# Kernel optimization log

Hardware: AMD Instinct MI355X
Metric: run time of the kernel (lower is better)

The kernel has to match this reference:

```python
import jax, jax.numpy as jnp
import numpy as np

N, IN_DIM, HEADS, OUT_DIM = 4096, 128, 4, 64
NEG_INF = -9.0e15  # finite mask value, matches torch source


def setup_inputs() -> dict:
    key = jax.random.key(0)
    k1, k2, k3, k4, k5 = jax.random.split(key, 5)
    x = jax.random.normal(k1, (N, IN_DIM), dtype=jnp.float32)
    adj_mask = jax.random.bernoulli(k2, 0.1, (N, N))  # bool, j->i edges
    # xavier-uniform-ish scales
    lim_w = float(np.sqrt(6.0 / (IN_DIM + HEADS * OUT_DIM)))
    W_lin = jax.random.uniform(k3, (IN_DIM, HEADS * OUT_DIM), minval=-lim_w, maxval=lim_w, dtype=jnp.float32)
    lim_a = float(np.sqrt(6.0 / (2 * OUT_DIM + 1)))
    a_src = jax.random.uniform(k4, (OUT_DIM,), minval=-lim_a, maxval=lim_a, dtype=jnp.float32)
    a_dst = jax.random.uniform(k5, (OUT_DIM,), minval=-lim_a, maxval=lim_a, dtype=jnp.float32)
    return {"x": x, "adj_mask": adj_mask, "W_lin": W_lin, "a_src": a_src, "a_dst": a_dst}


def reference(x, adj_mask, W_lin, a_src, a_dst):
    n = x.shape[0]
    h = (x @ W_lin).reshape(n, HEADS, OUT_DIM)           # (N, H, D)
    # att(cat(h_i, h_j)) decomposes linearly: a_src.h_i + a_dst.h_j
    s_i = jnp.einsum("nhd,d->nh", h, a_src)              # (N, H) contribution of dest node i
    s_j = jnp.einsum("nhd,d->nh", h, a_dst)              # (N, H) contribution of source node j
    e = jax.nn.leaky_relu(s_i[:, None, :] + s_j[None, :, :], 0.2)  # (N, N, H)
    e = jnp.where(adj_mask[:, :, None], e, NEG_INF)
    attn = jax.nn.softmax(e, axis=1)                     # softmax over source nodes j
    out = jnp.einsum("ijh,jhd->ihd", attn, h)            # per-head aggregation
    return out.reshape(n, HEADS * OUT_DIM)               # concat=True
```

## Files before the change

### kernel.cpp

```cpp
#include <hip/hip_runtime.h>
#include <math.h>


#define N 4096
#define IN_DIM 128
#define HEADS 4
#define OUT_DIM 64
#define HD 256
#define LOG2E 1.4426950408889634f
#define PSHIFT 8.0f

typedef _Float16 f16x8 __attribute__((ext_vector_type(8)));
typedef __fp16 fp16x2 __attribute__((ext_vector_type(2)));
typedef float f32x4 __attribute__((ext_vector_type(4)));

union F16x8u { fp16x2 h2[4]; f16x8 v; };

#define WS_HB_OFF    0u
#define WS_SSRC_OFF  2097152u
#define WS_SDT_OFF   2162688u
#define WS_BITT_OFF  2228224u
#define WS_HSUM_OFF  4325376u
#define WS_PL_OFF    4329472u
#define WS_PART_OFF  5242880u
#define WS_NEED8     (5242880u + 8u * 4194304u)
#define WS_NEED2     (5242880u + 2u * 4194304u)

__device__ __forceinline__ float lrelu(float v) { return fmaxf(v, 0.2f * v); }

__device__ __forceinline__ unsigned pack_bytes(unsigned v) {
  return (v & 1u) | ((v >> 7) & 2u) | ((v >> 14) & 4u) | ((v >> 21) & 8u);
}

__global__ __launch_bounds__(256) void prep_k(const void* __restrict__ mraw,
                                              unsigned* __restrict__ bits_t,
                                              const float* __restrict__ x,
                                              const float* __restrict__ W,
                                              const float* __restrict__ a_src,
                                              const float* __restrict__ a_dst,
                                              _Float16* __restrict__ hb,
                                              float* __restrict__ s_src,
                                              float* __restrict__ s_dst_t,
                                              float* __restrict__ hsum) {
  if (blockIdx.x < 2048) {
    __shared__ int s_flag;
    if (threadIdx.x == 0) s_flag = 0;
    __syncthreads();
    const unsigned* mw = (const unsigned*)mraw;
    int bad = 0, g = 0;
    for (int i = threadIdx.x; i < 1024; i += 256) {
      unsigned v = mw[i];
      if (v & 0xFEFEFEFEu) bad = 1;
      if (v > 1u) g = 1;
    }
    if (bad || g) atomicOr(&s_flag, (bad ? 1 : 0) | (g ? 2 : 0));
    __syncthreads();
    const bool byte_fmt = ((s_flag & 1) == 0) && ((s_flag & 2) != 0);

    int w = blockIdx.x * 256 + threadIdx.x;
    unsigned ob = 0u;
    if (byte_fmt) {
      const uint4* p = (const uint4*)((const unsigned char*)mraw + (size_t)w * 32u);
      uint4 a = p[0], b = p[1];
      ob  =  pack_bytes(a.x)        | (pack_bytes(a.y) << 4)  | (pack_bytes(a.z) << 8)  | (pack_bytes(a.w) << 12);
      ob |= (pack_bytes(b.x) << 16) | (pack_bytes(b.y) << 20) | (pack_bytes(b.z) << 24) | (pack_bytes(b.w) << 28);
    } else {
      const uint4* p = (const uint4*)((const unsigned*)mraw + (size_t)w * 32u);
#pragma unroll
      for (int k = 0; k < 8; ++k) {
        uint4 v = p[k];
        ob |= (v.x ? 1u : 0u) << (4 * k);
        ob |= (v.y ? 1u : 0u) << (4 * k + 1);
        ob |= (v.z ? 1u : 0u) << (4 * k + 2);
        ob |= (v.w ? 1u : 0u) << (4 * k + 3);
      }
    }
    const int row = w >> 7, jc = w & 127;
    bits_t[((size_t)(row >> 6) * 128 + jc) * 64 + (row & 63)] = ob;
  } else {
    const int i0 = (blockIdx.x - 2048) * 8;
    const int c = threadIdx.x;

    float acc[8];
#pragma unroll
    for (int r = 0; r < 8; ++r) acc[r] = 0.f;

    for (int kk = 0; kk < IN_DIM / 4; ++kk) {
      const int k = kk * 4;
      float w0 = W[(size_t)(k + 0) * HD + c];
      float w1 = W[(size_t)(k + 1) * HD + c];
      float w2 = W[(size_t)(k + 2) * HD + c];
      float w3 = W[(size_t)(k + 3) * HD + c];
#pragma unroll
      for (int r = 0; r < 8; ++r) {
        float4 xv = *(const float4*)(x + (size_t)(i0 + r) * IN_DIM + k);
        acc[r] = fmaf(xv.x, w0, fmaf(xv.y, w1, fmaf(xv.z, w2, fmaf(xv.w, w3, acc[r]))));
      }
    }

    {
      const int head = c >> 6, nt = (c >> 4) & 3, m15 = c & 15;
      const int unit = (head * 128 + (i0 >> 5)) * 4 + nt;
      const int lanep = ((i0 & 31) >> 3) * 16 + m15;
      f16x8 v;
#pragma unroll
      for (int r = 0; r < 8; ++r) v[r] = (_Float16)acc[r];
      *(f16x8*)(hb + (size_t)unit * 512 + lanep * 8) = v;
    }

    {
      float loc = 0.f;
#pragma unroll
      for (int r = 0; r < 8; ++r) loc += acc[r];
      atomicAdd(&hsum[c], loc);
    }

    const int hw = c >> 6, lane = c & 63;
    const float as = a_src[lane], ad = a_dst[lane];
#pragma unroll
    for (int r = 0; r < 8; ++r) {
      float vs = acc[r] * as, vd = acc[r] * ad;
#pragma unroll
      for (int off = 1; off < 64; off <<= 1) {
        vs += __shfl_xor(vs, off);
        vd += __shfl_xor(vd, off);
      }
      if (lane == 0) {
        s_src[(size_t)(i0 + r) * HEADS + hw] = vs * LOG2E;
        s_dst_t[(size_t)hw * N + (i0 + r)] = vd * LOG2E;
      }
    }
  }
}

__global__ __launch_bounds__(512, 4) void gat_aggr(const _Float16* __restrict__ hb,
                                                   const float* __restrict__ s_src,
                                                   const float* __restrict__ s_dst_t,
                                                   const unsigned* __restrict__ bits_t,
                                                   float* __restrict__ accp,
                                                   float* __restrict__ lp,
                                                   int jshift) {
  const int jsplit = 1 << jshift;
  const int jrange = N >> jshift;
  const int chunks = jrange >> 5;
  const int tid = threadIdx.x;
  const int wave = tid >> 6;
  const int lane = tid & 63;
  const int head = wave & 3;
  const int mg = wave >> 2;
  const int m15 = lane & 15;
  const int quad = lane >> 4;
  const int jq = blockIdx.x & (jsplit - 1);
  const int it = blockIdx.x >> jshift;
  const int i0 = it * 64;
  const int rA = i0 + mg * 32 + m15;
  const int rB = rA + 16;

  const float siA = s_src[(size_t)rA * HEADS + head];
  const float siB = s_src[(size_t)rB * HEADS + head];

  const unsigned* mt = bits_t + ((size_t)it * 128 + jq * chunks) * 64 + mg * 32 + m15;
  const float* sjb = s_dst_t + (size_t)head * N + jq * jrange + quad * 8;
  const _Float16* hbp = hb + ((size_t)(head * 128 + jq * chunks) * 4) * 512 + lane * 8;

  f32x4 accA0 = {0.f, 0.f, 0.f, 0.f}, accA1 = accA0, accA2 = accA0, accA3 = accA0;
  f32x4 accB0 = accA0, accB1 = accA0, accB2 = accA0, accB3 = accA0;
  float lA = 0.f, lB = 0.f;

  const int shq = quad * 8;

  for (int c = 0; c < chunks; ++c) {
    const unsigned mwA = mt[c * 64];
    const unsigned mwB = mt[c * 64 + 16];
    const float4 sa = *(const float4*)(sjb + c * 32);
    const float4 sb = *(const float4*)(sjb + c * 32 + 4);

    const f16x8 b0 = *(const f16x8*)(hbp + (size_t)(c * 4 + 0) * 512);
    const f16x8 b1 = *(const f16x8*)(hbp + (size_t)(c * 4 + 1) * 512);
    const f16x8 b2 = *(const f16x8*)(hbp + (size_t)(c * 4 + 2) * 512);
    const f16x8 b3 = *(const f16x8*)(hbp + (size_t)(c * 4 + 3) * 512);

    const unsigned wA = mwA >> shq;
    const unsigned wB = mwB >> shq;
    const float sjs[8] = {sa.x, sa.y, sa.z, sa.w, sb.x, sb.y, sb.z, sb.w};

    F16x8u uA, uB;
#pragma unroll
    for (int t2 = 0; t2 < 4; ++t2) {
      float pA[2], pB[2];
#pragma unroll
      for (int q = 0; q < 2; ++q) {
        const int t = t2 * 2 + q;
        const float sj = sjs[t];
        float vA = lrelu(siA + sj);
        float vB = lrelu(siB + sj);
        float xA = (((wA >> t) & 1u) ? vA : -1.0e38f) - PSHIFT;
        float xB = (((wB >> t) & 1u) ? vB : -1.0e38f) - PSHIFT;
        pA[q] = __builtin_amdgcn_exp2f(xA);
        pB[q] = __builtin_amdgcn_exp2f(xB);
        lA += pA[q];
        lB += pB[q];
      }
      uA.h2[t2] = __builtin_amdgcn_cvt_pkrtz(pA[0], pA[1]);
      uB.h2[t2] = __builtin_amdgcn_cvt_pkrtz(pB[0], pB[1]);
    }

    accA0 = __builtin_amdgcn_mfma_f32_16x16x32_f16(uA.v, b0, accA0, 0, 0, 0);
    accA1 = __builtin_amdgcn_mfma_f32_16x16x32_f16(uA.v, b1, accA1, 0, 0, 0);
    accA2 = __builtin_amdgcn_mfma_f32_16x16x32_f16(uA.v, b2, accA2, 0, 0, 0);
    accA3 = __builtin_amdgcn_mfma_f32_16x16x32_f16(uA.v, b3, accA3, 0, 0, 0);
    accB0 = __builtin_amdgcn_mfma_f32_16x16x32_f16(uB.v, b0, accB0, 0, 0, 0);
    accB1 = __builtin_amdgcn_mfma_f32_16x16x32_f16(uB.v, b1, accB1, 0, 0, 0);
    accB2 = __builtin_amdgcn_mfma_f32_16x16x32_f16(uB.v, b2, accB2, 0, 0, 0);
    accB3 = __builtin_amdgcn_mfma_f32_16x16x32_f16(uB.v, b3, accB3, 0, 0, 0);
  }

  lA += __shfl_xor(lA, 16); lA += __shfl_xor(lA, 32);
  lB += __shfl_xor(lB, 16); lB += __shfl_xor(lB, 32);
  if (quad == 0) {
    lp[((size_t)jq * N + rA) * HEADS + head] = lA;
    lp[((size_t)jq * N + rB) * HEADS + head] = lB;
  }

  const int colb = head * 64 + m15;
  float* oA = accp + (size_t)jq * (N * HD) + (size_t)(i0 + mg * 32 + quad * 4) * HD + colb;
  float* oB = oA + (size_t)16 * HD;
#pragma unroll
  for (int reg = 0; reg < 4; ++reg) {
    oA[(size_t)reg * HD + 0]  = accA0[reg];
    oA[(size_t)reg * HD + 16] = accA1[reg];
    oA[(size_t)reg * HD + 32] = accA2[reg];
    oA[(size_t)reg * HD + 48] = accA3[reg];
    oB[(size_t)reg * HD + 0]  = accB0[reg];
    oB[(size_t)reg * HD + 16] = accB1[reg];
    oB[(size_t)reg * HD + 32] = accB2[reg];
    oB[(size_t)reg * HD + 48] = accB3[reg];
  }
}

__global__ __launch_bounds__(256) void reduce_part(const float4* __restrict__ accp,
                                                   const float* __restrict__ lp,
                                                   const float* __restrict__ hsum,
                                                   float4* __restrict__ out, int jsplit) {
  const size_t idx = (size_t)blockIdx.x * 256 + threadIdx.x;
  const int row = (int)(idx >> 6);
  const int col4 = (int)(idx & 63);
  const int head = col4 >> 4;
  const size_t S = (size_t)N * HD / 4;

  float4 o = accp[idx];
  float lt = lp[(size_t)row * HEADS + head];
  for (int k = 1; k < jsplit; ++k) {
    float4 a = accp[idx + (size_t)k * S];
    o.x += a.x; o.y += a.y; o.z += a.z; o.w += a.w;
    lt += lp[((size_t)k * N + row) * HEADS + head];
  }
  if (lt == 0.f) {
    float4 hs = ((const float4*)hsum)[col4];
    const float c = 1.0f / (float)N;
    o.x = hs.x * c; o.y = hs.y * c; o.z = hs.z * c; o.w = hs.w * c;
  } else {
    const float inv = 1.0f / lt;
    o.x *= inv; o.y *= inv; o.z *= inv; o.w *= inv;
  }
  out[idx] = o;
}

extern "C" void kernel_launch(void* const* d_in, const int* in_sizes, int n_in,
                              void* d_out, int out_size, void* d_ws, size_t ws_size,
                              hipStream_t stream) {
  (void)in_sizes; (void)n_in; (void)out_size;
  const float* x = (const float*)d_in[0];
  const void* mask = d_in[1];
  const float* W = (const float*)d_in[2];
  const float* a_src = (const float*)d_in[3];
  const float* a_dst = (const float*)d_in[4];
  float* out = (float*)d_out;

  char* ws = (char*)d_ws;
  _Float16* hb = (_Float16*)(ws + WS_HB_OFF);
  float* s_src = (float*)(ws + WS_SSRC_OFF);
  float* s_dst_t = (float*)(ws + WS_SDT_OFF);
  unsigned* bits_t = (unsigned*)(ws + WS_BITT_OFF);
  float* hsum = (float*)(ws + WS_HSUM_OFF);
  float* lp = (float*)(ws + WS_PL_OFF);
  float* accp = (float*)(ws + WS_PART_OFF);

  const int jshift = (ws_size >= (size_t)WS_NEED8) ? 3 : 1;
  const int jsplit = 1 << jshift;

  (void)hipMemsetAsync(hsum, 0, HD * sizeof(float), stream);
  prep_k<<<2048 + N / 8, 256, 0, stream>>>(mask, bits_t, x, W, a_src, a_dst,
                                           hb, s_src, s_dst_t, hsum);
  gat_aggr<<<(N / 64) * jsplit, 512, 0, stream>>>(hb, s_src, s_dst_t, bits_t,
                                                  accp, lp, jshift);
  reduce_part<<<(N * HD / 4) / 256, 256, 0, stream>>>((const float4*)accp, lp, hsum,
                                                      (float4*)out, jsplit);
}
```

Measured before the change: 163.5 us.

## Split prep kernel, stage x in LDS, replace hsum atomics with partial sums

The combined prep kernel is split into a mask-packing kernel and a separate projection kernel. The projection kernel stages its 8 rows of x in shared memory. The global atomicAdd into hsum is replaced by per-block partial sums that reduce_part adds up only for rows with no edges, which also removes the memset launch. This drops the memset and the atomic contention but adds a kernel launch, loses overlap between mask packing and the projection, and makes isolated rows loop over 512 partial sums.

```diff
diff --git a/kernel.cpp b/kernel.cpp
--- a/kernel.cpp
+++ b/kernel.cpp
@@ -20,11 +20,11 @@
 #define WS_SSRC_OFF  2097152u
 #define WS_SDT_OFF   2162688u
 #define WS_BITT_OFF  2228224u
-#define WS_HSUM_OFF  4325376u
-#define WS_PL_OFF    4329472u
-#define WS_PART_OFF  5242880u
-#define WS_NEED8     (5242880u + 8u * 4194304u)
-#define WS_NEED2     (5242880u + 2u * 4194304u)
+#define WS_HSUMP_OFF 4325376u
+#define WS_PL_OFF    4849664u
+#define WS_PART_OFF  5373952u
+#define WS_NEED8     (5373952u + 8u * 4194304u)
+#define WS_NEED2     (5373952u + 2u * 4194304u)
 
 __device__ __forceinline__ float lrelu(float v) { return fmaxf(v, 0.2f * v); }
 
@@ -32,103 +32,106 @@
   return (v & 1u) | ((v >> 7) & 2u) | ((v >> 14) & 4u) | ((v >> 21) & 8u);
 }
 
-__global__ __launch_bounds__(256) void prep_k(const void* __restrict__ mraw,
-                                              unsigned* __restrict__ bits_t,
-                                              const float* __restrict__ x,
-                                              const float* __restrict__ W,
-                                              const float* __restrict__ a_src,
-                                              const float* __restrict__ a_dst,
-                                              _Float16* __restrict__ hb,
-                                              float* __restrict__ s_src,
-                                              float* __restrict__ s_dst_t,
-                                              float* __restrict__ hsum) {
-  if (blockIdx.x < 2048) {
-    __shared__ int s_flag;
-    if (threadIdx.x == 0) s_flag = 0;
-    __syncthreads();
-    const unsigned* mw = (const unsigned*)mraw;
-    int bad = 0, g = 0;
-    for (int i = threadIdx.x; i < 1024; i += 256) {
-      unsigned v = mw[i];
-      if (v & 0xFEFEFEFEu) bad = 1;
-      if (v > 1u) g = 1;
-    }
-    if (bad || g) atomicOr(&s_flag, (bad ? 1 : 0) | (g ? 2 : 0));
-    __syncthreads();
-    const bool byte_fmt = ((s_flag & 1) == 0) && ((s_flag & 2) != 0);
-
-    int w = blockIdx.x * 256 + threadIdx.x;
-    unsigned ob = 0u;
-    if (byte_fmt) {
-      const uint4* p = (const uint4*)((const unsigned char*)mraw + (size_t)w * 32u);
-      uint4 a = p[0], b = p[1];
-      ob  =  pack_bytes(a.x)        | (pack_bytes(a.y) << 4)  | (pack_bytes(a.z) << 8)  | (pack_bytes(a.w) << 12);
-      ob |= (pack_bytes(b.x) << 16) | (pack_bytes(b.y) << 20) | (pack_bytes(b.z) << 24) | (pack_bytes(b.w) << 28);
-    } else {
-      const uint4* p = (const uint4*)((const unsigned*)mraw + (size_t)w * 32u);
-#pragma unroll
-      for (int k = 0; k < 8; ++k) {
-        uint4 v = p[k];
-        ob |= (v.x ? 1u : 0u) << (4 * k);
-        ob |= (v.y ? 1u : 0u) << (4 * k + 1);
-        ob |= (v.z ? 1u : 0u) << (4 * k + 2);
-        ob |= (v.w ? 1u : 0u) << (4 * k + 3);
-      }
-    }
-    const int row = w >> 7, jc = w & 127;
-    bits_t[((size_t)(row >> 6) * 128 + jc) * 64 + (row & 63)] = ob;
+__global__ __launch_bounds__(256) void pack_mask_k(const void* __restrict__ mraw,
+                                                   unsigned* __restrict__ bits_t) {
+  __shared__ int s_flag;
+  if (threadIdx.x == 0) s_flag = 0;
+  __syncthreads();
+  const unsigned* mw = (const unsigned*)mraw;
+  int bad = 0, g = 0;
+  for (int i = threadIdx.x; i < 1024; i += 256) {
+    unsigned v = mw[i];
+    if (v & 0xFEFEFEFEu) bad = 1;
+    if (v > 1u) g = 1;
+  }
+  if (bad || g) atomicOr(&s_flag, (bad ? 1 : 0) | (g ? 2 : 0));
+  __syncthreads();
+  const bool byte_fmt = ((s_flag & 1) == 0) && ((s_flag & 2) != 0);
+
+  int w = blockIdx.x * 256 + threadIdx.x;
+  unsigned ob = 0u;
+  if (byte_fmt) {
+    const uint4* p = (const uint4*)((const unsigned char*)mraw + (size_t)w * 32u);
+    uint4 a = p[0], b = p[1];
+    ob  =  pack_bytes(a.x)        | (pack_bytes(a.y) << 4)  | (pack_bytes(a.z) << 8)  | (pack_bytes(a.w) << 12);
+    ob |= (pack_bytes(b.x) << 16) | (pack_bytes(b.y) << 20) | (pack_bytes(b.z) << 24) | (pack_bytes(b.w) << 28);
   } else {
-    const int i0 = (blockIdx.x - 2048) * 8;
-    const int c = threadIdx.x;
-
-    float acc[8];
-#pragma unroll
-    for (int r = 0; r < 8; ++r) acc[r] = 0.f;
-
-    for (int kk = 0; kk < IN_DIM / 4; ++kk) {
-      const int k = kk * 4;
-      float w0 = W[(size_t)(k + 0) * HD + c];
-      float w1 = W[(size_t)(k + 1) * HD + c];
-      float w2 = W[(size_t)(k + 2) * HD + c];
-      float w3 = W[(size_t)(k + 3) * HD + c];
-#pragma unroll
-      for (int r = 0; r < 8; ++r) {
-        float4 xv = *(const float4*)(x + (size_t)(i0 + r) * IN_DIM + k);
-        acc[r] = fmaf(xv.x, w0, fmaf(xv.y, w1, fmaf(xv.z, w2, fmaf(xv.w, w3, acc[r]))));
-      }
-    }
-
-    {
-      const int head = c >> 6, nt = (c >> 4) & 3, m15 = c & 15;
-      const int unit = (head * 128 + (i0 >> 5)) * 4 + nt;
-      const int lanep = ((i0 & 31) >> 3) * 16 + m15;
-      f16x8 v;
-#pragma unroll
-      for (int r = 0; r < 8; ++r) v[r] = (_Float16)acc[r];
-      *(f16x8*)(hb + (size_t)unit * 512 + lanep * 8) = v;
-    }
-
-    {
-      float loc = 0.f;
-#pragma unroll
-      for (int r = 0; r < 8; ++r) loc += acc[r];
-      atomicAdd(&hsum[c], loc);
-    }
-
-    const int hw = c >> 6, lane = c & 63;
-    const float as = a_src[lane], ad = a_dst[lane];
+    const uint4* p = (const uint4*)((const unsigned*)mraw + (size_t)w * 32u);
+#pragma unroll
+    for (int k = 0; k < 8; ++k) {
+      uint4 v = p[k];
+      ob |= (v.x ? 1u : 0u) << (4 * k);
+      ob |= (v.y ? 1u : 0u) << (4 * k + 1);
+      ob |= (v.z ? 1u : 0u) << (4 * k + 2);
+      ob |= (v.w ? 1u : 0u) << (4 * k + 3);
+    }
+  }
+  const int row = w >> 7, jc = w & 127;
+  bits_t[((size_t)(row >> 6) * 128 + jc) * 64 + (row & 63)] = ob;
+}
+
+__global__ __launch_bounds__(256) void compute_h(const float* __restrict__ x,
+                                                 const float* __restrict__ W,
+                                                 const float* __restrict__ a_src,
+                                                 const float* __restrict__ a_dst,
+                                                 _Float16* __restrict__ hb,
+                                                 float* __restrict__ s_src,
+                                                 float* __restrict__ s_dst_t,
+                                                 float* __restrict__ hsum_part) {
+  __shared__ float xs[8][IN_DIM];
+  const int i0 = blockIdx.x * 8;
+  const int c = threadIdx.x;
+
+  ((float4*)&xs[0][0])[c] = ((const float4*)(x + (size_t)i0 * IN_DIM))[c];
+  __syncthreads();
+
+  float acc[8];
+#pragma unroll
+  for (int r = 0; r < 8; ++r) acc[r] = 0.f;
+
+  for (int kk = 0; kk < IN_DIM / 4; ++kk) {
+    const int k = kk * 4;
+    float w0 = W[(size_t)(k + 0) * HD + c];
+    float w1 = W[(size_t)(k + 1) * HD + c];
+    float w2 = W[(size_t)(k + 2) * HD + c];
+    float w3 = W[(size_t)(k + 3) * HD + c];
 #pragma unroll
     for (int r = 0; r < 8; ++r) {
-      float vs = acc[r] * as, vd = acc[r] * ad;
-#pragma unroll
-      for (int off = 1; off < 64; off <<= 1) {
-        vs += __shfl_xor(vs, off);
-        vd += __shfl_xor(vd, off);
-      }
-      if (lane == 0) {
-        s_src[(size_t)(i0 + r) * HEADS + hw] = vs * LOG2E;
-        s_dst_t[(size_t)hw * N + (i0 + r)] = vd * LOG2E;
-      }
+      float4 xv = *(const float4*)(&xs[r][k]);
+      acc[r] = fmaf(xv.x, w0, fmaf(xv.y, w1, fmaf(xv.z, w2, fmaf(xv.w, w3, acc[r]))));
+    }
+  }
+
+  {
+    const int head = c >> 6, nt = (c >> 4) & 3, m15 = c & 15;
+    const int unit = (head * 128 + (i0 >> 5)) * 4 + nt;
+    const int lanep = ((i0 & 31) >> 3) * 16 + m15;
+    f16x8 v;
+#pragma unroll
+    for (int r = 0; r < 8; ++r) v[r] = (_Float16)acc[r];
+    *(f16x8*)(hb + (size_t)unit * 512 + lanep * 8) = v;
+  }
+
+  {
+    float loc = 0.f;
+#pragma unroll
+    for (int r = 0; r < 8; ++r) loc += acc[r];
+    hsum_part[(size_t)blockIdx.x * HD + c] = loc;
+  }
+
+  const int hw = c >> 6, lane = c & 63;
+  const float as = a_src[lane], ad = a_dst[lane];
+#pragma unroll
+  for (int r = 0; r < 8; ++r) {
+    float vs = acc[r] * as, vd = acc[r] * ad;
+#pragma unroll
+    for (int off = 1; off < 64; off <<= 1) {
+      vs += __shfl_xor(vs, off);
+      vd += __shfl_xor(vd, off);
+    }
+    if (lane == 0) {
+      s_src[(size_t)(i0 + r) * HEADS + hw] = vs * LOG2E;
+      s_dst_t[(size_t)hw * N + (i0 + r)] = vd * LOG2E;
     }
   }
 }
@@ -240,7 +243,7 @@
 
 __global__ __launch_bounds__(256) void reduce_part(const float4* __restrict__ accp,
                                                    const float* __restrict__ lp,
-                                                   const float* __restrict__ hsum,
+                                                   const float* __restrict__ hsum_part,
                                                    float4* __restrict__ out, int jsplit) {
   const size_t idx = (size_t)blockIdx.x * 256 + threadIdx.x;
   const int row = (int)(idx >> 6);
@@ -256,9 +259,13 @@
     lt += lp[((size_t)k * N + row) * HEADS + head];
   }
   if (lt == 0.f) {
-    float4 hs = ((const float4*)hsum)[col4];
-    const float c = 1.0f / (float)N;
-    o.x = hs.x * c; o.y = hs.y * c; o.z = hs.z * c; o.w = hs.w * c;
+    float4 hs = {0.f, 0.f, 0.f, 0.f};
+    for (int b = 0; b < 512; ++b) {
+      float4 t = ((const float4*)hsum_part)[(size_t)b * 64 + col4];
+      hs.x += t.x; hs.y += t.y; hs.z += t.z; hs.w += t.w;
+    }
+    const float cst = 1.0f / (float)N;
+    o.x = hs.x * cst; o.y = hs.y * cst; o.z = hs.z * cst; o.w = hs.w * cst;
   } else {
     const float inv = 1.0f / lt;
     o.x *= inv; o.y *= inv; o.z *= inv; o.w *= inv;
@@ -282,18 +289,17 @@
   float* s_src = (float*)(ws + WS_SSRC_OFF);
   float* s_dst_t = (float*)(ws + WS_SDT_OFF);
   unsigned* bits_t = (unsigned*)(ws + WS_BITT_OFF);
-  float* hsum = (float*)(ws + WS_HSUM_OFF);
+  float* hsum_part = (float*)(ws + WS_HSUMP_OFF);
   float* lp = (float*)(ws + WS_PL_OFF);
   float* accp = (float*)(ws + WS_PART_OFF);
 
   const int jshift = (ws_size >= (size_t)WS_NEED8) ? 3 : 1;
   const int jsplit = 1 << jshift;
 
-  (void)hipMemsetAsync(hsum, 0, HD * sizeof(float), stream);
-  prep_k<<<2048 + N / 8, 256, 0, stream>>>(mask, bits_t, x, W, a_src, a_dst,
-                                           hb, s_src, s_dst_t, hsum);
+  pack_mask_k<<<(N * N / 32) / 256, 256, 0, stream>>>(mask, bits_t);
+  compute_h<<<N / 8, 256, 0, stream>>>(x, W, a_src, a_dst, hb, s_src, s_dst_t, hsum_part);
   gat_aggr<<<(N / 64) * jsplit, 512, 0, stream>>>(hb, s_src, s_dst_t, bits_t,
                                                   accp, lp, jshift);
-  reduce_part<<<(N * HD / 4) / 256, 256, 0, stream>>>((const float4*)accp, lp, hsum,
+  reduce_part<<<(N * HD / 4) / 256, 256, 0, stream>>>((const float4*)accp, lp, hsum_part,
                                                       (float4*)out, jsplit);
 }
```

Measured after the change: 153.4 us. 6.2% less time.
